# Optimization experiments

Hardware: AMD Instinct MI355X
Metric: run time of the kernel (lower is better)

Reference implementation:

```python
import jax, jax.numpy as jnp
import numpy as np

IOU_THRESHOLD = 0.5
EPS = 1e-7  # ultralytics bbox_iou eps


def _bbox_iou_xywh(b1, b2):
    # b1, b2: broadcastable [..., 4] in (cx, cy, w, h) format (ultralytics default xywh=True)
    x1, y1, w1, h1 = b1[..., 0], b1[..., 1], b1[..., 2], b1[..., 3]
    x2, y2, w2, h2 = b2[..., 0], b2[..., 1], b2[..., 2], b2[..., 3]
    b1x1, b1x2 = x1 - w1 * 0.5, x1 + w1 * 0.5
    b1y1, b1y2 = y1 - h1 * 0.5, y1 + h1 * 0.5
    b2x1, b2x2 = x2 - w2 * 0.5, x2 + w2 * 0.5
    b2y1, b2y2 = y2 - h2 * 0.5, y2 + h2 * 0.5
    iw = jnp.clip(jnp.minimum(b1x2, b2x2) - jnp.maximum(b1x1, b2x1), 0.0)
    ih = jnp.clip(jnp.minimum(b1y2, b2y2) - jnp.maximum(b1y1, b2y1), 0.0)
    inter = iw * ih
    union = w1 * h1 + w2 * h2 - inter + EPS
    return inter / union


def setup_inputs() -> dict:
    key = jax.random.key(0)
    k1, k2, k3, k4, k5 = jax.random.split(key, 5)
    N, R, M, C = 2048, 10, 2048, 84
    xy = jax.random.uniform(k1, (N, 2), minval=0.0, maxval=1000.0)
    wh = jax.random.uniform(k2, (N, 2), minval=30.0, maxval=80.0)
    boxes = jnp.concatenate([xy, wh], axis=-1)                      # [N, 4] xywh
    pred = jnp.concatenate([boxes, jax.random.uniform(k3, (N, C - 4))], axis=-1)  # [N, C]
    # dropout runs: same boxes with ~1px jitter -> IoU > 0.5 guaranteed (realistic MC-dropout)
    dropout_preds = boxes[None, :, :] + jax.random.normal(k4, (R, M, 4))          # [R, M, 4]
    dropout_cls_confs = jax.nn.softmax(jax.random.normal(k5, (R, M, C)), axis=-1)  # [R, M, C]
    return {"pred": pred, "dropout_preds": dropout_preds, "dropout_cls_confs": dropout_cls_confs}


def reference(pred, dropout_preds, dropout_cls_confs):
    # pred: [N, C] (first 4 cols = xywh box); dropout_preds: [R, M, 4]; dropout_cls_confs: [R, M, C]
    R = dropout_preds.shape[0]
    iou = _bbox_iou_xywh(pred[:, None, None, :4], dropout_preds[None, :, :, :])  # [N, R, M]
    hit = iou > IOU_THRESHOLD                                                    # [N, R, M]
    matched = jnp.any(hit, axis=-1)                                              # [N, R]
    first_idx = jnp.argmax(hit, axis=-1)                                         # first j with iou>thr (torch break)
    # gather cls confidences of the first match per (pred, run): [N, R, C]
    conf = dropout_cls_confs[jnp.arange(R)[None, :], first_idx]
    # runs without a match contribute nothing to the entropy sum; p=1 -> -p*log(p)=0
    p = jnp.where(matched[..., None], conf, 1.0)
    entropy = -(p * jnp.log(p)).sum(axis=1)                                      # [N, C], sum over matched runs
    # faithful to torch: zero fallback row gives 0*log(0)=nan entropy
    entropy = jnp.where(jnp.any(matched, axis=1)[:, None], entropy, jnp.nan)
    sm = jax.nn.softmax(entropy, axis=-1)                                        # softmax over classes
    return (1.0 - sm).max(axis=-1)                                               # [N]
```

## Files before the change

### kernel.cpp

```cpp
#include <hip/hip_runtime.h>
#include <math.h>

#define NN 2048
#define RR 10
#define MM 2048
#define CC 84
#define IEPS 1e-7f

__global__ __launch_bounds__(640) void fused_kernel(
    const float* __restrict__ pred,
    const float* __restrict__ dpreds,
    const float* __restrict__ confs,
    float* __restrict__ out) {
  __shared__ int sidx[RR];

  const int n = blockIdx.x;
  const int r = threadIdx.x >> 6;
  const int lane = threadIdx.x & 63;

  float4 pb = *reinterpret_cast<const float4*>(pred + (size_t)n * CC);
  const float b1x1 = fmaf(-0.5f, pb.z, pb.x), b1x2 = fmaf(0.5f, pb.z, pb.x);
  const float b1y1 = fmaf(-0.5f, pb.w, pb.y), b1y2 = fmaf(0.5f, pb.w, pb.y);
  const float a1e = pb.z * pb.w + IEPS;

  const float4* __restrict__ dp =
      reinterpret_cast<const float4*>(dpreds + (size_t)r * MM * 4);

  int found = -1;
  for (int m0 = 0; m0 < MM; m0 += 256) {
    float4 d0 = dp[m0 + lane];
    float4 d1 = dp[m0 + 64 + lane];
    float4 d2 = dp[m0 + 128 + lane];
    float4 d3 = dp[m0 + 192 + lane];

#define HIT(db, h)                                                          \
    {                                                                       \
      float x1 = fmaf(-0.5f, db.z, db.x), x2 = fmaf(0.5f, db.z, db.x);      \
      float y1 = fmaf(-0.5f, db.w, db.y), y2 = fmaf(0.5f, db.w, db.y);      \
      float iw = fmaxf(fminf(b1x2, x2) - fmaxf(b1x1, x1), 0.0f);            \
      float ih = fmaxf(fminf(b1y2, y2) - fmaxf(b1y1, y1), 0.0f);            \
      float inter = iw * ih;                                                \
      float t = fmaf(db.z, db.w, a1e);                   \
      h = (3.0f * inter > t);                                               \
    }
    bool h0, h1, h2, h3;
    HIT(d0, h0) HIT(d1, h1) HIT(d2, h2) HIT(d3, h3)
#undef HIT

    unsigned long long b0 = __ballot(h0);
    unsigned long long b1 = __ballot(h1);
    unsigned long long b2 = __ballot(h2);
    unsigned long long b3 = __ballot(h3);
    if (b0 | b1 | b2 | b3) {
      if (b0)      found = m0 +       (__ffsll(b0) - 1);
      else if (b1) found = m0 + 64  + (__ffsll(b1) - 1);
      else if (b2) found = m0 + 128 + (__ffsll(b2) - 1);
      else         found = m0 + 192 + (__ffsll(b3) - 1);
      break;
    }
  }
  if (lane == 0) sidx[r] = found;
  __syncthreads();

  if (r == 0) {
    int idxs[RR];
    bool anym = false;
#pragma unroll
    for (int q = 0; q < RR; ++q) {
      idxs[q] = sidx[q];
      anym = anym || (idxs[q] >= 0);
    }

    const bool has_hi = (lane + 64) < CC;
    float e0 = 0.0f, e1 = 0.0f;
#pragma unroll
    for (int q = 0; q < RR; ++q) {
      if (idxs[q] >= 0) {
        const float* row = confs + ((size_t)q * MM + (size_t)idxs[q]) * CC;
        float p0 = row[lane];
        e0 -= p0 * __logf(p0);
        if (has_hi) {
          float p1 = row[lane + 64];
          e1 -= p1 * __logf(p1);
        }
      }
    }

    float maxE = fmaxf(e0, has_hi ? e1 : -INFINITY);
    float minE = fminf(e0, has_hi ? e1 : INFINITY);
#pragma unroll
    for (int o = 32; o >= 1; o >>= 1) {
      maxE = fmaxf(maxE, __shfl_xor(maxE, o));
      minE = fminf(minE, __shfl_xor(minE, o));
    }
    float s = __expf(e0 - maxE) + (has_hi ? __expf(e1 - maxE) : 0.0f);
#pragma unroll
    for (int o = 32; o >= 1; o >>= 1) s += __shfl_xor(s, o);

    float result = anym ? (1.0f - __expf(minE - maxE) / s) : nanf("");
    if (lane == 0) out[n] = result;
  }
}

extern "C" void kernel_launch(void* const* d_in, const int* in_sizes, int n_in,
                              void* d_out, int out_size, void* d_ws, size_t ws_size,
                              hipStream_t stream) {
  const float* pred   = (const float*)d_in[0];
  const float* dpreds = (const float*)d_in[1];
  const float* confs  = (const float*)d_in[2];
  float* out = (float*)d_out;

  fused_kernel<<<NN, 640, 0, stream>>>(pred, dpreds, confs, out);
}
```

Baseline: 23.93 us.

## Process four predictions per block, reusing each dropout box load

Each block now handles four prediction boxes instead of one. Every loaded dropout box is tested against all four, so the dpreds traffic and the per-box corner math are shared across them. The scan now advances 64 boxes per step with a one-step register prefetch and stops once all four predictions have a match. Blocks are remapped with a multiplicative permutation to spread work, and four waves do the entropy/softmax epilogue. The cost is a quarter as many blocks (less parallelism) and the loop running until the slowest of the four finds its match.

Measured after the change: 25.38 us. +6.1%, slower.

```diff
diff --git a/kernel.cpp b/kernel.cpp
--- a/kernel.cpp
+++ b/kernel.cpp
@@ -6,76 +6,83 @@
 #define MM 2048
 #define CC 84
 #define IEPS 1e-7f
+#define FINF 0x7fffffff
 
 __global__ __launch_bounds__(640) void fused_kernel(
     const float* __restrict__ pred,
     const float* __restrict__ dpreds,
     const float* __restrict__ confs,
     float* __restrict__ out) {
-  __shared__ int sidx[RR];
+  __shared__ int sidx[4 * RR];
 
-  const int n = blockIdx.x;
+  const int b = blockIdx.x;
+  const int g = (b * 171) & 511;
   const int r = threadIdx.x >> 6;
   const int lane = threadIdx.x & 63;
+  const int nb = g << 2;
 
-  float4 pb = *reinterpret_cast<const float4*>(pred + (size_t)n * CC);
-  const float b1x1 = fmaf(-0.5f, pb.z, pb.x), b1x2 = fmaf(0.5f, pb.z, pb.x);
-  const float b1y1 = fmaf(-0.5f, pb.w, pb.y), b1y2 = fmaf(0.5f, pb.w, pb.y);
-  const float a1e = pb.z * pb.w + IEPS;
+  float bx1[4], bx2[4], by1[4], by2[4], a1e[4];
+#pragma unroll
+  for (int i = 0; i < 4; ++i) {
+    float4 pb = *reinterpret_cast<const float4*>(pred + (size_t)(nb + i) * CC);
+    bx1[i] = fmaf(-0.5f, pb.z, pb.x);
+    bx2[i] = fmaf(0.5f, pb.z, pb.x);
+    by1[i] = fmaf(-0.5f, pb.w, pb.y);
+    by2[i] = fmaf(0.5f, pb.w, pb.y);
+    a1e[i] = pb.z * pb.w + IEPS;
+  }
 
   const float4* __restrict__ dp =
       reinterpret_cast<const float4*>(dpreds + (size_t)r * MM * 4);
 
-  int found = -1;
-  for (int m0 = 0; m0 < MM; m0 += 256) {
-    float4 d0 = dp[m0 + lane];
-    float4 d1 = dp[m0 + 64 + lane];
-    float4 d2 = dp[m0 + 128 + lane];
-    float4 d3 = dp[m0 + 192 + lane];
+  int f0 = FINF, f1 = FINF, f2 = FINF, f3 = FINF;
+  float4 cur = dp[lane];
+  for (int m0 = 0; m0 < MM; m0 += 64) {
+    float4 nxt = cur;
+    if (m0 + 64 < MM) nxt = dp[m0 + 64 + lane];
 
-#define HIT(db, h)                                                          \
+    float x1 = fmaf(-0.5f, cur.z, cur.x), x2 = fmaf(0.5f, cur.z, cur.x);
+    float y1 = fmaf(-0.5f, cur.w, cur.y), y2 = fmaf(0.5f, cur.w, cur.y);
+    float a2 = cur.z * cur.w;
+
+#define TEST(i, f)                                                          \
     {                                                                       \
-      float x1 = fmaf(-0.5f, db.z, db.x), x2 = fmaf(0.5f, db.z, db.x);      \
-      float y1 = fmaf(-0.5f, db.w, db.y), y2 = fmaf(0.5f, db.w, db.y);      \
-      float iw = fmaxf(fminf(b1x2, x2) - fmaxf(b1x1, x1), 0.0f);            \
-      float ih = fmaxf(fminf(b1y2, y2) - fmaxf(b1y1, y1), 0.0f);            \
+      float iw = fmaxf(fminf(bx2[i], x2) - fmaxf(bx1[i], x1), 0.0f);        \
+      float ih = fmaxf(fminf(by2[i], y2) - fmaxf(by1[i], y1), 0.0f);        \
       float inter = iw * ih;                                                \
-      float t = fmaf(db.z, db.w, a1e);                   \
-      h = (3.0f * inter > t);                                               \
+      float t = a2 + a1e[i];                                                \
+      unsigned long long bal = __ballot(3.0f * inter > t);                  \
+      int cand = bal ? (m0 + __ffsll(bal) - 1) : FINF;                      \
+      f = min(f, cand);                                                     \
     }
-    bool h0, h1, h2, h3;
-    HIT(d0, h0) HIT(d1, h1) HIT(d2, h2) HIT(d3, h3)
-#undef HIT
+    TEST(0, f0) TEST(1, f1) TEST(2, f2) TEST(3, f3)
+#undef TEST
 
-    unsigned long long b0 = __ballot(h0);
-    unsigned long long b1 = __ballot(h1);
-    unsigned long long b2 = __ballot(h2);
-    unsigned long long b3 = __ballot(h3);
-    if (b0 | b1 | b2 | b3) {
-      if (b0)      found = m0 +       (__ffsll(b0) - 1);
-      else if (b1) found = m0 + 64  + (__ffsll(b1) - 1);
-      else if (b2) found = m0 + 128 + (__ffsll(b2) - 1);
-      else         found = m0 + 192 + (__ffsll(b3) - 1);
-      break;
-    }
+    if (max(max(f0, f1), max(f2, f3)) != FINF) break;
+    cur = nxt;
   }
-  if (lane == 0) sidx[r] = found;
+  if (lane == 0) {
+    sidx[0 * RR + r] = f0;
+    sidx[1 * RR + r] = f1;
+    sidx[2 * RR + r] = f2;
+    sidx[3 * RR + r] = f3;
+  }
   __syncthreads();
 
-  if (r == 0) {
+  if (r < 4) {
     int idxs[RR];
     bool anym = false;
 #pragma unroll
     for (int q = 0; q < RR; ++q) {
-      idxs[q] = sidx[q];
-      anym = anym || (idxs[q] >= 0);
+      idxs[q] = sidx[r * RR + q];
+      anym = anym || (idxs[q] < MM);
     }
 
     const bool has_hi = (lane + 64) < CC;
     float e0 = 0.0f, e1 = 0.0f;
 #pragma unroll
     for (int q = 0; q < RR; ++q) {
-      if (idxs[q] >= 0) {
+      if (idxs[q] < MM) {
         const float* row = confs + ((size_t)q * MM + (size_t)idxs[q]) * CC;
         float p0 = row[lane];
         e0 -= p0 * __logf(p0);
@@ -98,7 +105,7 @@
     for (int o = 32; o >= 1; o >>= 1) s += __shfl_xor(s, o);
 
     float result = anym ? (1.0f - __expf(minE - maxE) / s) : nanf("");
-    if (lane == 0) out[n] = result;
+    if (lane == 0) out[nb + r] = result;
   }
 }
 
@@ -110,5 +117,5 @@
   const float* confs  = (const float*)d_in[2];
   float* out = (float*)d_out;
 
-  fused_kernel<<<NN, 640, 0, stream>>>(pred, dpreds, confs, out);
+  fused_kernel<<<NN / 4, 640, 0, stream>>>(pred, dpreds, confs, out);
 }
```
